# Kernel optimization log

Hardware: AMD Instinct MI355X
Metric: run time of the kernel (lower is better)

The kernel has to match this reference:

```python
import jax, jax.numpy as jnp
import numpy as np

H, D, TS, A, R, TR = 256, 2, 32, 4, 16, 8  # h_size, max_output_degree, t_size, n_aggr, rank, t_rank
BS = 16384


def setup_inputs() -> dict:
    key = jax.random.key(0)
    ks = jax.random.split(key, 9)
    return {
        "neighbour_h": jax.random.normal(ks[0], (BS, D, H), jnp.float32),
        "type_embs": jax.random.normal(ks[1], (BS, TS), jnp.float32),
        # per-child input projections U: (max_output_degree, n_aggr, h_size, rank)
        "U": jax.random.normal(ks[2], (D, A, H, R), jnp.float32) * 0.05,
        "b": jax.random.normal(ks[3], (D, A, 1, R), jnp.float32) * 0.05,
        # type projection
        "U_type": jax.random.normal(ks[4], (TS, A * TR), jnp.float32) * 0.05,
        "b_type": jax.random.normal(ks[5], (1, A * TR), jnp.float32) * 0.05,
        # stacked augmented core tensors T_list: (n_aggr, t_rank+1, rank+1, rank+1, rank)
        "T": jax.random.normal(ks[6], (A, TR + 1, R + 1, R + 1, R), jnp.float32) * 0.02,
        # output projection
        "U_output": jax.random.normal(ks[7], (A, R, H), jnp.float32) * 0.05,
        "b_output": jax.random.normal(ks[8], (A, 1, H), jnp.float32) * 0.05,
    }


def _aug(x):
    # append a constant-1 feature along the last dim: (bs, a, d) -> (bs, a, d+1)
    bs, a, _ = x.shape
    return jnp.concatenate([x, jnp.ones((bs, a, 1), x.dtype)], axis=-1)


def reference(neighbour_h, type_embs, U, b, U_type, b_type, T, U_output, b_output):
    # child projections: (bs, n_ch, n_aggr, rank)
    ch = jnp.einsum('bch,cahr->bcar', neighbour_h, U) + b[:, :, 0, :]
    # type projection: (bs, n_aggr, t_rank)
    tp = (type_embs @ U_type + b_type).reshape(-1, A, TR)
    # augmented (homogeneous) inputs
    h0 = _aug(tp)         # (bs, a, TR+1)
    h1 = _aug(ch[:, 0])   # (bs, a, R+1)
    h2 = _aug(ch[:, 1])   # (bs, a, R+1)
    # sequential multilinear (Tucker/HOSVD) contraction with the core tensor,
    # vectorized over batch and aggregators (original loops over n_aggr)
    r = jnp.einsum('bap,apqrs->baqrs', h0, T)
    r = jnp.einsum('baq,baqrs->bars', h1, r)
    g = jnp.einsum('bar,bars->bas', h2, r)            # (bs, a, R)
    out = jnp.einsum('bar,arh->bah', g, U_output) + b_output[:, 0, :]
    return out.reshape(neighbour_h.shape[0], -1)      # (bs, n_aggr*h_size)
```

## Files before the change

kernel.cpp:

```cpp
#include <hip/hip_runtime.h>

#define NTHR 512
#define TB 32

typedef __attribute__((ext_vector_type(8))) short bf16x8;
typedef __attribute__((ext_vector_type(16))) float f32x16;
typedef __attribute__((ext_vector_type(4))) float f32v4;
typedef float4 f4;
typedef unsigned short u16;

__device__ __forceinline__ u16 f2b(float x) {
  union { float f; unsigned u; } v; v.f = x;
  unsigned r = (v.u + 0x7fffu + ((v.u >> 16) & 1u)) >> 16;
  return (u16)r;
}
__device__ __forceinline__ float b2f(u16 u) {
  union { unsigned u; float f; } v; v.u = ((unsigned)u) << 16;
  return v.f;
}
__device__ __forceinline__ unsigned pack2(float a, float b) {
  return (unsigned)f2b(a) | ((unsigned)f2b(b) << 16);
}
__device__ __forceinline__ unsigned cvtpk(float lo, float hi) {
  unsigned r;
  asm("v_cvt_pk_bf16_f32 %0, %1, %2" : "=v"(r) : "v"(lo), "v"(hi));
  return r;
}
__device__ __forceinline__ f4 ntload4(const float* p) {
  f32v4 v = __builtin_nontemporal_load((const f32v4*)p);
  return make_float4(v.x, v.y, v.z, v.w);
}

#define MFMA32(A, B, C) __builtin_amdgcn_mfma_f32_32x32x16_bf16(A, B, C, 0, 0, 0)

extern "C" __global__ void hosvd_prep(const float* __restrict__ U,
                                      const float* __restrict__ T,
                                      const float* __restrict__ UO,
                                      unsigned* __restrict__ ws32) {
  int id = blockIdx.x * 256 + threadIdx.x;
  if (id < 102400) {
    int j2 = id & 3, frag = id >> 2;
    int l = frag & 63, f2 = frag >> 6;
    int nt = f2 % 5, aks = f2 / 5;
    int ks = aks % 20, a = aks / 20;
    int n = nt * 32 + (l & 31);
    int p = n >> 4, s = n & 15;
    float v[2];
    #pragma unroll
    for (int j = 0; j < 2; ++j) {
      int kp = ks * 16 + (l >> 5) * 8 + j2 * 2 + j;
      int q = (unsigned)kp / 18u, r = kp - q * 18;
      float x = 0.f;
      if (p <= 8 && q <= 16 && r <= 16)
        x = T[(((a * 9 + p) * 17 + q) * 17 + r) * 16 + s];
      v[j] = x;
    }
    ws32[id] = pack2(v[0], v[1]);
  } else if (id < 118784) {
    int rel = id - 102400;
    int j2 = rel & 3, frag = rel >> 2;
    int l = frag & 63, f2 = frag >> 6;
    int nt = f2 & 1, ks = (f2 >> 1) & 15, c = f2 >> 5;
    int n = nt * 32 + (l & 31);
    int a = n >> 4, rr = n & 15;
    int k = ks * 16 + (l >> 5) * 8 + j2 * 2;
    float v0 = U[((c * 4 + a) * 256 + k + 0) * 16 + rr];
    float v1 = U[((c * 4 + a) * 256 + k + 1) * 16 + rr];
    ws32[id] = pack2(v0, v1);
  } else if (id < 126976) {
    int rel = id - 118784;
    int j2 = rel & 3, frag = rel >> 2;
    int l = frag & 63, f2 = frag >> 6;
    int ht = f2 & 7, a = f2 >> 3;
    int h = ht * 32 + (l & 31);
    int k = (l >> 5) * 8 + j2 * 2;
    float v0 = UO[(a * 16 + k + 0) * 256 + h];
    float v1 = UO[(a * 16 + k + 1) * 256 + h];
    ws32[id] = pack2(v0, v1);
  }
}

extern "C" __global__ __launch_bounds__(NTHR, 4)
void hosvd_main(const float* __restrict__ nh, const float* __restrict__ te,
                const float* __restrict__ bw, const float* __restrict__ Ut,
                const float* __restrict__ bt, const float* __restrict__ bO,
                const u16* __restrict__ BTf, const u16* __restrict__ UcTf,
                const u16* __restrict__ UOTf, float* __restrict__ out) {
  __shared__ __align__(16) u16   s_u[20800];
  __shared__ __align__(16) u16   s_ch[TB * 164];
  __shared__ __align__(16) float s_tpt[36 * 32];

  const int t = threadIdx.x;
  const int ib0 = blockIdx.x * TB;
  const int w = t >> 6, l = t & 63;
  const int l31 = l & 31, hi = l >> 5;

  float* UtL = (float*)&s_u[16640];
  float* teL = (float*)&s_u[18688];
  float* s_redf = (float*)s_u;

  if (t < 256) {
    const int row = t >> 3, cc = (t >> 2) & 1, aa = t & 3;
    *(uint2*)&s_ch[row * 164 + cc * 80 + aa * 20 + 16] = make_uint2(0x3F80u, 0u);
  }
  if (t < 128) {
    const int aa = t >> 5, row = t & 31;
    s_tpt[(aa * 9 + 8) * 32 + row] = 1.0f;
  }

  if (t < 256) {
    const int row = t >> 3, k4 = t & 7;
    f4 v = ntload4(&te[(size_t)(ib0 + row) * 32 + k4 * 4]);
    float* d = &teL[row * 33 + k4 * 4];
    d[0] = v.x; d[1] = v.y; d[2] = v.z; d[3] = v.w;
  } else {
    const int j = t - 256;
    *(f4*)&UtL[j * 4] = *(const f4*)&Ut[j * 4];
  }
  for (int lp = t; lp < 4096; lp += NTHR) {
    const int row = lp >> 7, rem = lp & 127;
    const int c = rem >> 6, k0 = (rem & 63) * 4;
    f4 v = ntload4(&nh[((size_t)(ib0 + row) * 2 + c) * 256 + k0]);
    *(uint2*)&s_u[row * 520 + c * 256 + k0] =
        make_uint2(cvtpk(v.x, v.y), cvtpk(v.z, v.w));
  }
  __syncthreads();

  if (w < 4) {
    const int c = w & 1, nt2 = w >> 1;
    f32x16 accC = {0.f, 0.f, 0.f, 0.f, 0.f, 0.f, 0.f, 0.f,
                   0.f, 0.f, 0.f, 0.f, 0.f, 0.f, 0.f, 0.f};
    #pragma unroll
    for (int ks = 0; ks < 16; ++ks) {
      bf16x8 Av = *(const bf16x8*)&s_u[l31 * 520 + c * 256 + ks * 16 + hi * 8];
      bf16x8 Bv = *(const bf16x8*)
          &UcTf[(size_t)(((c * 16 + ks) * 2 + nt2) * 64 + l) * 8];
      accC = MFMA32(Av, Bv, accC);
    }
    const int n = nt2 * 32 + l31;
    const int ca = n >> 4, rr = n & 15;
    const float bias = bw[(c * 4 + ca) * 16 + rr];
    #pragma unroll
    for (int reg = 0; reg < 16; ++reg) {
      const int row = (reg & 3) + 8 * (reg >> 2) + 4 * hi;
      s_ch[row * 164 + c * 80 + ca * 20 + rr] = f2b(accC[reg] + bias);
    }
  } else {
    const int t2 = t - 256;
    const int i = t2 >> 3, off = (t2 & 7) * 4;
    float ac0 = bt[off], ac1 = bt[off + 1], ac2 = bt[off + 2], ac3 = bt[off + 3];
    #pragma unroll
    for (int k = 0; k < 32; ++k) {
      const float tv = teL[i * 33 + k];
      f4 u = *(const f4*)&UtL[k * 32 + off];
      ac0 = fmaf(tv, u.x, ac0);
      ac1 = fmaf(tv, u.y, ac1);
      ac2 = fmaf(tv, u.z, ac2);
      ac3 = fmaf(tv, u.w, ac3);
    }
    #pragma unroll
    for (int jj = 0; jj < 4; ++jj) {
      const int o2 = off + jj;
      const float v = (jj == 0) ? ac0 : (jj == 1) ? ac1 : (jj == 2) ? ac2 : ac3;
      s_tpt[((o2 >> 3) * 9 + (o2 & 7)) * 32 + i] = v;
    }
  }
  __syncthreads();

  {
    const int a = w & 3, kh = w >> 2;
    const u16* h1g = &s_ch[l31 * 164 + a * 20];
    const u16* h2g = h1g + 80;

    f32x16 acc[5];
    #pragma unroll
    for (int nt = 0; nt < 5; ++nt)
      acc[nt] = (f32x16){0.f, 0.f, 0.f, 0.f, 0.f, 0.f, 0.f, 0.f,
                         0.f, 0.f, 0.f, 0.f, 0.f, 0.f, 0.f, 0.f};

    __builtin_amdgcn_s_setprio(1);
    #pragma unroll
    for (int ks2 = 0; ks2 < 10; ++ks2) {
      const int ks = kh * 10 + ks2;
      const u16* bp = &BTf[(size_t)((a * 20 + ks) * 5) * 512 + l * 8];
      bf16x8 B0 = *(const bf16x8*)(bp + 0 * 512);
      bf16x8 B1 = *(const bf16x8*)(bp + 1 * 512);
      bf16x8 B2 = *(const bf16x8*)(bp + 2 * 512);
      bf16x8 B3 = *(const bf16x8*)(bp + 3 * 512);
      bf16x8 B4 = *(const bf16x8*)(bp + 4 * 512);

      const int k0 = ks * 16 + hi * 8;
      const unsigned q0 = (unsigned)k0 / 18u;
      const int r0 = k0 - (int)q0 * 18;
      const int brk = 18 - r0;
      const float h1a = b2f(h1g[q0]);
      const float h1b = b2f(h1g[q0 + 1]);
      float hv[8];
      #pragma unroll
      for (int j = 0; j < 8; ++j) {
        int rr = r0 + j;
        rr = (rr >= 18) ? rr - 18 : rr;
        const float h2v = b2f(h2g[rr]);
        hv[j] = ((j < brk) ? h1a : h1b) * h2v;
      }
      union { unsigned u[4]; bf16x8 v; } Au;
      Au.u[0] = cvtpk(hv[0], hv[1]);
      Au.u[1] = cvtpk(hv[2], hv[3]);
      Au.u[2] = cvtpk(hv[4], hv[5]);
      Au.u[3] = cvtpk(hv[6], hv[7]);

      acc[0] = MFMA32(Au.v, B0, acc[0]);
      acc[1] = MFMA32(Au.v, B1, acc[1]);
      acc[2] = MFMA32(Au.v, B2, acc[2]);
      acc[3] = MFMA32(Au.v, B3, acc[3]);
      acc[4] = MFMA32(Au.v, B4, acc[4]);
    }
    __builtin_amdgcn_s_setprio(0);

    float gp[16];
    #pragma unroll
    for (int reg = 0; reg < 16; ++reg) gp[reg] = 0.f;
    #pragma unroll
    for (int nt = 0; nt < 5; ++nt) {
      int pp = nt * 2 + (l31 >> 4);
      if (pp > 8) pp = 8;
      const float* tpb = &s_tpt[(a * 9 + pp) * 32 + 4 * hi];
      f4 t0 = *(const f4*)&tpb[0];
      f4 t1 = *(const f4*)&tpb[8];
      f4 t2 = *(const f4*)&tpb[16];
      f4 t3 = *(const f4*)&tpb[24];
      gp[0]  = fmaf(t0.x, acc[nt][0],  gp[0]);
      gp[1]  = fmaf(t0.y, acc[nt][1],  gp[1]);
      gp[2]  = fmaf(t0.z, acc[nt][2],  gp[2]);
      gp[3]  = fmaf(t0.w, acc[nt][3],  gp[3]);
      gp[4]  = fmaf(t1.x, acc[nt][4],  gp[4]);
      gp[5]  = fmaf(t1.y, acc[nt][5],  gp[5]);
      gp[6]  = fmaf(t1.z, acc[nt][6],  gp[6]);
      gp[7]  = fmaf(t1.w, acc[nt][7],  gp[7]);
      gp[8]  = fmaf(t2.x, acc[nt][8],  gp[8]);
      gp[9]  = fmaf(t2.y, acc[nt][9],  gp[9]);
      gp[10] = fmaf(t2.z, acc[nt][10], gp[10]);
      gp[11] = fmaf(t2.w, acc[nt][11], gp[11]);
      gp[12] = fmaf(t3.x, acc[nt][12], gp[12]);
      gp[13] = fmaf(t3.y, acc[nt][13], gp[13]);
      gp[14] = fmaf(t3.z, acc[nt][14], gp[14]);
      gp[15] = fmaf(t3.w, acc[nt][15], gp[15]);
    }
    #pragma unroll
    for (int reg = 0; reg < 16; ++reg)
      gp[reg] += __shfl_xor(gp[reg], 16, 64);
    if ((l & 16) == 0) {
      const int s = l & 15;
      #pragma unroll
      for (int reg = 0; reg < 16; ++reg) {
        const int row = (reg & 3) + 8 * (reg >> 2) + 4 * hi;
        s_redf[((kh * 4 + a) * 32 + row) * 16 + s] = gp[reg];
      }
    }
  }
  __syncthreads();

  {
    #pragma unroll
    for (int a = 0; a < 4; ++a) {
      const float* r0p = &s_redf[((0 + a) * 32 + l31) * 16 + hi * 8];
      const float* r1p = &s_redf[((4 + a) * 32 + l31) * 16 + hi * 8];
      f4 xa = *(const f4*)&r0p[0], xb = *(const f4*)&r0p[4];
      f4 ya = *(const f4*)&r1p[0], yb = *(const f4*)&r1p[4];
      union { unsigned u[4]; bf16x8 v; } Au;
      Au.u[0] = cvtpk(xa.x + ya.x, xa.y + ya.y);
      Au.u[1] = cvtpk(xa.z + ya.z, xa.w + ya.w);
      Au.u[2] = cvtpk(xb.x + yb.x, xb.y + yb.y);
      Au.u[3] = cvtpk(xb.z + yb.z, xb.w + yb.w);
      bf16x8 Bv = *(const bf16x8*)&UOTf[((size_t)(a * 8 + w) * 64 + l) * 8];
      const int h = w * 32 + l31;
      const float bias = bO[a * 256 + h];
      f32x16 accE = {bias, bias, bias, bias, bias, bias, bias, bias,
                     bias, bias, bias, bias, bias, bias, bias, bias};
      accE = MFMA32(Au.v, Bv, accE);
      #pragma unroll
      for (int reg = 0; reg < 16; ++reg) {
        const int row = (reg & 3) + 8 * (reg >> 2) + 4 * hi;
        __builtin_nontemporal_store(
            accE[reg], &out[(size_t)(ib0 + row) * 1024 + a * 256 + h]);
      }
    }
  }
}

extern "C" void kernel_launch(void* const* d_in, const int* in_sizes, int n_in,
                              void* d_out, int out_size, void* d_ws, size_t ws_size,
                              hipStream_t stream) {
  const float* nh = (const float*)d_in[0];
  const float* te = (const float*)d_in[1];
  const float* U  = (const float*)d_in[2];
  const float* bw = (const float*)d_in[3];
  const float* Ut = (const float*)d_in[4];
  const float* bt = (const float*)d_in[5];
  const float* T  = (const float*)d_in[6];
  const float* UO = (const float*)d_in[7];
  const float* bO = (const float*)d_in[8];
  float* out = (float*)d_out;

  unsigned* ws32 = (unsigned*)d_ws;
  hipLaunchKernelGGL(hosvd_prep, dim3(496), dim3(256), 0, stream, U, T, UO, ws32);

  const u16* BTf  = (const u16*)d_ws;
  const u16* UcTf = BTf + 204800;
  const u16* UOTf = UcTf + 32768;

  const int bs = in_sizes[0] / 512;
  hipLaunchKernelGGL(hosvd_main, dim3(bs / TB), dim3(NTHR), 0, stream,
                     nh, te, bw, Ut, bt, bO, BTf, UcTf, UOTf, out);
}
```

Baseline: 39.49 us.

## Process two batch tiles per block with register prefetch of second tile

Each block now handles two 32-row tiles (the second offset by half the batch), halving the grid. After the first tile's projection phase, the second tile's neighbour and type inputs are loaded into registers so the global load latency overlaps the first tile's core contraction and output stage. Launch bounds drop from 4 to 2 blocks per SM to make room for the 8 extra float4 prefetch registers. This trades occupancy and grid parallelism (256 blocks) for latency hiding.

After: 79.74 us. +101.9%, slower.

```diff
diff --git a/kernel.cpp b/kernel.cpp
--- a/kernel.cpp
+++ b/kernel.cpp
@@ -80,18 +80,18 @@
   }
 }
 
-extern "C" __global__ __launch_bounds__(NTHR, 4)
+extern "C" __global__ __launch_bounds__(NTHR, 2)
 void hosvd_main(const float* __restrict__ nh, const float* __restrict__ te,
                 const float* __restrict__ bw, const float* __restrict__ Ut,
                 const float* __restrict__ bt, const float* __restrict__ bO,
                 const u16* __restrict__ BTf, const u16* __restrict__ UcTf,
-                const u16* __restrict__ UOTf, float* __restrict__ out) {
+                const u16* __restrict__ UOTf, float* __restrict__ out,
+                int half) {
   __shared__ __align__(16) u16   s_u[20800];
   __shared__ __align__(16) u16   s_ch[TB * 164];
   __shared__ __align__(16) float s_tpt[36 * 32];
 
   const int t = threadIdx.x;
-  const int ib0 = blockIdx.x * TB;
   const int w = t >> 6, l = t & 63;
   const int l31 = l & 31, hi = l >> 5;
 
@@ -108,183 +108,221 @@
     s_tpt[(aa * 9 + 8) * 32 + row] = 1.0f;
   }
 
-  if (t < 256) {
-    const int row = t >> 3, k4 = t & 7;
-    f4 v = ntload4(&te[(size_t)(ib0 + row) * 32 + k4 * 4]);
-    float* d = &teL[row * 33 + k4 * 4];
-    d[0] = v.x; d[1] = v.y; d[2] = v.z; d[3] = v.w;
-  } else {
-    const int j = t - 256;
-    *(f4*)&UtL[j * 4] = *(const f4*)&Ut[j * 4];
-  }
-  for (int lp = t; lp < 4096; lp += NTHR) {
-    const int row = lp >> 7, rem = lp & 127;
-    const int c = rem >> 6, k0 = (rem & 63) * 4;
-    f4 v = ntload4(&nh[((size_t)(ib0 + row) * 2 + c) * 256 + k0]);
-    *(uint2*)&s_u[row * 520 + c * 256 + k0] =
-        make_uint2(cvtpk(v.x, v.y), cvtpk(v.z, v.w));
-  }
-  __syncthreads();
-
-  if (w < 4) {
-    const int c = w & 1, nt2 = w >> 1;
-    f32x16 accC = {0.f, 0.f, 0.f, 0.f, 0.f, 0.f, 0.f, 0.f,
-                   0.f, 0.f, 0.f, 0.f, 0.f, 0.f, 0.f, 0.f};
-    #pragma unroll
-    for (int ks = 0; ks < 16; ++ks) {
-      bf16x8 Av = *(const bf16x8*)&s_u[l31 * 520 + c * 256 + ks * 16 + hi * 8];
-      bf16x8 Bv = *(const bf16x8*)
-          &UcTf[(size_t)(((c * 16 + ks) * 2 + nt2) * 64 + l) * 8];
-      accC = MFMA32(Av, Bv, accC);
-    }
-    const int n = nt2 * 32 + l31;
-    const int ca = n >> 4, rr = n & 15;
-    const float bias = bw[(c * 4 + ca) * 16 + rr];
-    #pragma unroll
-    for (int reg = 0; reg < 16; ++reg) {
-      const int row = (reg & 3) + 8 * (reg >> 2) + 4 * hi;
-      s_ch[row * 164 + c * 80 + ca * 20 + rr] = f2b(accC[reg] + bias);
-    }
-  } else {
-    const int t2 = t - 256;
-    const int i = t2 >> 3, off = (t2 & 7) * 4;
-    float ac0 = bt[off], ac1 = bt[off + 1], ac2 = bt[off + 2], ac3 = bt[off + 3];
-    #pragma unroll
-    for (int k = 0; k < 32; ++k) {
-      const float tv = teL[i * 33 + k];
-      f4 u = *(const f4*)&UtL[k * 32 + off];
-      ac0 = fmaf(tv, u.x, ac0);
-      ac1 = fmaf(tv, u.y, ac1);
-      ac2 = fmaf(tv, u.z, ac2);
-      ac3 = fmaf(tv, u.w, ac3);
-    }
-    #pragma unroll
-    for (int jj = 0; jj < 4; ++jj) {
-      const int o2 = off + jj;
-      const float v = (jj == 0) ? ac0 : (jj == 1) ? ac1 : (jj == 2) ? ac2 : ac3;
-      s_tpt[((o2 >> 3) * 9 + (o2 & 7)) * 32 + i] = v;
-    }
-  }
-  __syncthreads();
-
-  {
-    const int a = w & 3, kh = w >> 2;
-    const u16* h1g = &s_ch[l31 * 164 + a * 20];
-    const u16* h2g = h1g + 80;
-
-    f32x16 acc[5];
-    #pragma unroll
-    for (int nt = 0; nt < 5; ++nt)
-      acc[nt] = (f32x16){0.f, 0.f, 0.f, 0.f, 0.f, 0.f, 0.f, 0.f,
-                         0.f, 0.f, 0.f, 0.f, 0.f, 0.f, 0.f, 0.f};
-
-    __builtin_amdgcn_s_setprio(1);
-    #pragma unroll
-    for (int ks2 = 0; ks2 < 10; ++ks2) {
-      const int ks = kh * 10 + ks2;
-      const u16* bp = &BTf[(size_t)((a * 20 + ks) * 5) * 512 + l * 8];
-      bf16x8 B0 = *(const bf16x8*)(bp + 0 * 512);
-      bf16x8 B1 = *(const bf16x8*)(bp + 1 * 512);
-      bf16x8 B2 = *(const bf16x8*)(bp + 2 * 512);
-      bf16x8 B3 = *(const bf16x8*)(bp + 3 * 512);
-      bf16x8 B4 = *(const bf16x8*)(bp + 4 * 512);
-
-      const int k0 = ks * 16 + hi * 8;
-      const unsigned q0 = (unsigned)k0 / 18u;
-      const int r0 = k0 - (int)q0 * 18;
-      const int brk = 18 - r0;
-      const float h1a = b2f(h1g[q0]);
-      const float h1b = b2f(h1g[q0 + 1]);
-      float hv[8];
-      #pragma unroll
-      for (int j = 0; j < 8; ++j) {
-        int rr = r0 + j;
-        rr = (rr >= 18) ? rr - 18 : rr;
-        const float h2v = b2f(h2g[rr]);
-        hv[j] = ((j < brk) ? h1a : h1b) * h2v;
-      }
-      union { unsigned u[4]; bf16x8 v; } Au;
-      Au.u[0] = cvtpk(hv[0], hv[1]);
-      Au.u[1] = cvtpk(hv[2], hv[3]);
-      Au.u[2] = cvtpk(hv[4], hv[5]);
-      Au.u[3] = cvtpk(hv[6], hv[7]);
-
-      acc[0] = MFMA32(Au.v, B0, acc[0]);
-      acc[1] = MFMA32(Au.v, B1, acc[1]);
-      acc[2] = MFMA32(Au.v, B2, acc[2]);
-      acc[3] = MFMA32(Au.v, B3, acc[3]);
-      acc[4] = MFMA32(Au.v, B4, acc[4]);
-    }
-    __builtin_amdgcn_s_setprio(0);
-
-    float gp[16];
-    #pragma unroll
-    for (int reg = 0; reg < 16; ++reg) gp[reg] = 0.f;
-    #pragma unroll
-    for (int nt = 0; nt < 5; ++nt) {
-      int pp = nt * 2 + (l31 >> 4);
-      if (pp > 8) pp = 8;
-      const float* tpb = &s_tpt[(a * 9 + pp) * 32 + 4 * hi];
-      f4 t0 = *(const f4*)&tpb[0];
-      f4 t1 = *(const f4*)&tpb[8];
-      f4 t2 = *(const f4*)&tpb[16];
-      f4 t3 = *(const f4*)&tpb[24];
-      gp[0]  = fmaf(t0.x, acc[nt][0],  gp[0]);
-      gp[1]  = fmaf(t0.y, acc[nt][1],  gp[1]);
-      gp[2]  = fmaf(t0.z, acc[nt][2],  gp[2]);
-      gp[3]  = fmaf(t0.w, acc[nt][3],  gp[3]);
-      gp[4]  = fmaf(t1.x, acc[nt][4],  gp[4]);
-      gp[5]  = fmaf(t1.y, acc[nt][5],  gp[5]);
-      gp[6]  = fmaf(t1.z, acc[nt][6],  gp[6]);
-      gp[7]  = fmaf(t1.w, acc[nt][7],  gp[7]);
-      gp[8]  = fmaf(t2.x, acc[nt][8],  gp[8]);
-      gp[9]  = fmaf(t2.y, acc[nt][9],  gp[9]);
-      gp[10] = fmaf(t2.z, acc[nt][10], gp[10]);
-      gp[11] = fmaf(t2.w, acc[nt][11], gp[11]);
-      gp[12] = fmaf(t3.x, acc[nt][12], gp[12]);
-      gp[13] = fmaf(t3.y, acc[nt][13], gp[13]);
-      gp[14] = fmaf(t3.z, acc[nt][14], gp[14]);
-      gp[15] = fmaf(t3.w, acc[nt][15], gp[15]);
-    }
-    #pragma unroll
-    for (int reg = 0; reg < 16; ++reg)
-      gp[reg] += __shfl_xor(gp[reg], 16, 64);
-    if ((l & 16) == 0) {
-      const int s = l & 15;
+  f4 Rnh[8];
+  f4 Rte;
+
+  for (int it = 0; it < 2; ++it) {
+    const int ib0 = blockIdx.x * TB + it * half;
+
+    if (it == 0) {
+      if (t < 256) {
+        const int row = t >> 3, k4 = t & 7;
+        f4 v = ntload4(&te[(size_t)(ib0 + row) * 32 + k4 * 4]);
+        float* d = &teL[row * 33 + k4 * 4];
+        d[0] = v.x; d[1] = v.y; d[2] = v.z; d[3] = v.w;
+      } else {
+        const int j = t - 256;
+        *(f4*)&UtL[j * 4] = *(const f4*)&Ut[j * 4];
+      }
+      for (int lp = t; lp < 4096; lp += NTHR) {
+        const int row = lp >> 7, rem = lp & 127;
+        const int c = rem >> 6, k0 = (rem & 63) * 4;
+        f4 v = ntload4(&nh[((size_t)(ib0 + row) * 2 + c) * 256 + k0]);
+        *(uint2*)&s_u[row * 520 + c * 256 + k0] =
+            make_uint2(cvtpk(v.x, v.y), cvtpk(v.z, v.w));
+      }
+    } else {
+      if (t < 256) {
+        const int row = t >> 3, k4 = t & 7;
+        float* d = &teL[row * 33 + k4 * 4];
+        d[0] = Rte.x; d[1] = Rte.y; d[2] = Rte.z; d[3] = Rte.w;
+      }
+      #pragma unroll
+      for (int k2 = 0; k2 < 8; ++k2) {
+        const int lp = t + k2 * NTHR;
+        const int row = lp >> 7, rem = lp & 127;
+        const int c = rem >> 6, k0 = (rem & 63) * 4;
+        f4 v = Rnh[k2];
+        *(uint2*)&s_u[row * 520 + c * 256 + k0] =
+            make_uint2(cvtpk(v.x, v.y), cvtpk(v.z, v.w));
+      }
+    }
+    __syncthreads();
+
+    if (w < 4) {
+      const int c = w & 1, nt2 = w >> 1;
+      f32x16 accC = {0.f, 0.f, 0.f, 0.f, 0.f, 0.f, 0.f, 0.f,
+                     0.f, 0.f, 0.f, 0.f, 0.f, 0.f, 0.f, 0.f};
+      #pragma unroll
+      for (int ks = 0; ks < 16; ++ks) {
+        bf16x8 Av = *(const bf16x8*)&s_u[l31 * 520 + c * 256 + ks * 16 + hi * 8];
+        bf16x8 Bv = *(const bf16x8*)
+            &UcTf[(size_t)(((c * 16 + ks) * 2 + nt2) * 64 + l) * 8];
+        accC = MFMA32(Av, Bv, accC);
+      }
+      const int n = nt2 * 32 + l31;
+      const int ca = n >> 4, rr = n & 15;
+      const float bias = bw[(c * 4 + ca) * 16 + rr];
       #pragma unroll
       for (int reg = 0; reg < 16; ++reg) {
         const int row = (reg & 3) + 8 * (reg >> 2) + 4 * hi;
-        s_redf[((kh * 4 + a) * 32 + row) * 16 + s] = gp[reg];
-      }
-    }
-  }
-  __syncthreads();
-
-  {
-    #pragma unroll
-    for (int a = 0; a < 4; ++a) {
-      const float* r0p = &s_redf[((0 + a) * 32 + l31) * 16 + hi * 8];
-      const float* r1p = &s_redf[((4 + a) * 32 + l31) * 16 + hi * 8];
-      f4 xa = *(const f4*)&r0p[0], xb = *(const f4*)&r0p[4];
-      f4 ya = *(const f4*)&r1p[0], yb = *(const f4*)&r1p[4];
-      union { unsigned u[4]; bf16x8 v; } Au;
-      Au.u[0] = cvtpk(xa.x + ya.x, xa.y + ya.y);
-      Au.u[1] = cvtpk(xa.z + ya.z, xa.w + ya.w);
-      Au.u[2] = cvtpk(xb.x + yb.x, xb.y + yb.y);
-      Au.u[3] = cvtpk(xb.z + yb.z, xb.w + yb.w);
-      bf16x8 Bv = *(const bf16x8*)&UOTf[((size_t)(a * 8 + w) * 64 + l) * 8];
-      const int h = w * 32 + l31;
-      const float bias = bO[a * 256 + h];
-      f32x16 accE = {bias, bias, bias, bias, bias, bias, bias, bias,
-                     bias, bias, bias, bias, bias, bias, bias, bias};
-      accE = MFMA32(Au.v, Bv, accE);
-      #pragma unroll
-      for (int reg = 0; reg < 16; ++reg) {
-        const int row = (reg & 3) + 8 * (reg >> 2) + 4 * hi;
-        __builtin_nontemporal_store(
-            accE[reg], &out[(size_t)(ib0 + row) * 1024 + a * 256 + h]);
-      }
-    }
+        s_ch[row * 164 + c * 80 + ca * 20 + rr] = f2b(accC[reg] + bias);
+      }
+    } else {
+      const int t2 = t - 256;
+      const int i = t2 >> 3, off = (t2 & 7) * 4;
+      float ac0 = bt[off], ac1 = bt[off + 1], ac2 = bt[off + 2], ac3 = bt[off + 3];
+      #pragma unroll
+      for (int k = 0; k < 32; ++k) {
+        const float tv = teL[i * 33 + k];
+        f4 u = *(const f4*)&UtL[k * 32 + off];
+        ac0 = fmaf(tv, u.x, ac0);
+        ac1 = fmaf(tv, u.y, ac1);
+        ac2 = fmaf(tv, u.z, ac2);
+        ac3 = fmaf(tv, u.w, ac3);
+      }
+      #pragma unroll
+      for (int jj = 0; jj < 4; ++jj) {
+        const int o2 = off + jj;
+        const float v = (jj == 0) ? ac0 : (jj == 1) ? ac1 : (jj == 2) ? ac2 : ac3;
+        s_tpt[((o2 >> 3) * 9 + (o2 & 7)) * 32 + i] = v;
+      }
+    }
+    __syncthreads();
+
+    if (it == 0) {
+      const int ib1 = blockIdx.x * TB + half;
+      #pragma unroll
+      for (int k2 = 0; k2 < 8; ++k2) {
+        const int lp = t + k2 * NTHR;
+        const int row = lp >> 7, rem = lp & 127;
+        const int c = rem >> 6, k0 = (rem & 63) * 4;
+        Rnh[k2] = ntload4(&nh[((size_t)(ib1 + row) * 2 + c) * 256 + k0]);
+      }
+      if (t < 256)
+        Rte = ntload4(&te[(size_t)(ib1 + (t >> 3)) * 32 + (t & 7) * 4]);
+    }
+
+    {
+      const int a = w & 3, kh = w >> 2;
+      const u16* h1g = &s_ch[l31 * 164 + a * 20];
+      const u16* h2g = h1g + 80;
+
+      f32x16 acc[5];
+      #pragma unroll
+      for (int nt = 0; nt < 5; ++nt)
+        acc[nt] = (f32x16){0.f, 0.f, 0.f, 0.f, 0.f, 0.f, 0.f, 0.f,
+                           0.f, 0.f, 0.f, 0.f, 0.f, 0.f, 0.f, 0.f};
+
+      __builtin_amdgcn_s_setprio(1);
+      #pragma unroll
+      for (int ks2 = 0; ks2 < 10; ++ks2) {
+        const int ks = kh * 10 + ks2;
+        const u16* bp = &BTf[(size_t)((a * 20 + ks) * 5) * 512 + l * 8];
+        bf16x8 B0 = *(const bf16x8*)(bp + 0 * 512);
+        bf16x8 B1 = *(const bf16x8*)(bp + 1 * 512);
+        bf16x8 B2 = *(const bf16x8*)(bp + 2 * 512);
+        bf16x8 B3 = *(const bf16x8*)(bp + 3 * 512);
+        bf16x8 B4 = *(const bf16x8*)(bp + 4 * 512);
+
+        const int k0 = ks * 16 + hi * 8;
+        const unsigned q0 = (unsigned)k0 / 18u;
+        const int r0 = k0 - (int)q0 * 18;
+        const int brk = 18 - r0;
+        const float h1a = b2f(h1g[q0]);
+        const float h1b = b2f(h1g[q0 + 1]);
+        float hv[8];
+        #pragma unroll
+        for (int j = 0; j < 8; ++j) {
+          int rr = r0 + j;
+          rr = (rr >= 18) ? rr - 18 : rr;
+          const float h2v = b2f(h2g[rr]);
+          hv[j] = ((j < brk) ? h1a : h1b) * h2v;
+        }
+        union { unsigned u[4]; bf16x8 v; } Au;
+        Au.u[0] = cvtpk(hv[0], hv[1]);
+        Au.u[1] = cvtpk(hv[2], hv[3]);
+        Au.u[2] = cvtpk(hv[4], hv[5]);
+        Au.u[3] = cvtpk(hv[6], hv[7]);
+
+        acc[0] = MFMA32(Au.v, B0, acc[0]);
+        acc[1] = MFMA32(Au.v, B1, acc[1]);
+        acc[2] = MFMA32(Au.v, B2, acc[2]);
+        acc[3] = MFMA32(Au.v, B3, acc[3]);
+        acc[4] = MFMA32(Au.v, B4, acc[4]);
+      }
+      __builtin_amdgcn_s_setprio(0);
+
+      float gp[16];
+      #pragma unroll
+      for (int reg = 0; reg < 16; ++reg) gp[reg] = 0.f;
+      #pragma unroll
+      for (int nt = 0; nt < 5; ++nt) {
+        int pp = nt * 2 + (l31 >> 4);
+        if (pp > 8) pp = 8;
+        const float* tpb = &s_tpt[(a * 9 + pp) * 32 + 4 * hi];
+        f4 t0 = *(const f4*)&tpb[0];
+        f4 t1 = *(const f4*)&tpb[8];
+        f4 t2 = *(const f4*)&tpb[16];
+        f4 t3 = *(const f4*)&tpb[24];
+        gp[0]  = fmaf(t0.x, acc[nt][0],  gp[0]);
+        gp[1]  = fmaf(t0.y, acc[nt][1],  gp[1]);
+        gp[2]  = fmaf(t0.z, acc[nt][2],  gp[2]);
+        gp[3]  = fmaf(t0.w, acc[nt][3],  gp[3]);
+        gp[4]  = fmaf(t1.x, acc[nt][4],  gp[4]);
+        gp[5]  = fmaf(t1.y, acc[nt][5],  gp[5]);
+        gp[6]  = fmaf(t1.z, acc[nt][6],  gp[6]);
+        gp[7]  = fmaf(t1.w, acc[nt][7],  gp[7]);
+        gp[8]  = fmaf(t2.x, acc[nt][8],  gp[8]);
+        gp[9]  = fmaf(t2.y, acc[nt][9],  gp[9]);
+        gp[10] = fmaf(t2.z, acc[nt][10], gp[10]);
+        gp[11] = fmaf(t2.w, acc[nt][11], gp[11]);
+        gp[12] = fmaf(t3.x, acc[nt][12], gp[12]);
+        gp[13] = fmaf(t3.y, acc[nt][13], gp[13]);
+        gp[14] = fmaf(t3.z, acc[nt][14], gp[14]);
+        gp[15] = fmaf(t3.w, acc[nt][15], gp[15]);
+      }
+      #pragma unroll
+      for (int reg = 0; reg < 16; ++reg)
+        gp[reg] += __shfl_xor(gp[reg], 16, 64);
+      if ((l & 16) == 0) {
+        const int s = l & 15;
+        #pragma unroll
+        for (int reg = 0; reg < 16; ++reg) {
+          const int row = (reg & 3) + 8 * (reg >> 2) + 4 * hi;
+          s_redf[((kh * 4 + a) * 32 + row) * 16 + s] = gp[reg];
+        }
+      }
+    }
+    __syncthreads();
+
+    {
+      #pragma unroll
+      for (int a = 0; a < 4; ++a) {
+        const float* r0p = &s_redf[((0 + a) * 32 + l31) * 16 + hi * 8];
+        const float* r1p = &s_redf[((4 + a) * 32 + l31) * 16 + hi * 8];
+        f4 xa = *(const f4*)&r0p[0], xb = *(const f4*)&r0p[4];
+        f4 ya = *(const f4*)&r1p[0], yb = *(const f4*)&r1p[4];
+        union { unsigned u[4]; bf16x8 v; } Au;
+        Au.u[0] = cvtpk(xa.x + ya.x, xa.y + ya.y);
+        Au.u[1] = cvtpk(xa.z + ya.z, xa.w + ya.w);
+        Au.u[2] = cvtpk(xb.x + yb.x, xb.y + yb.y);
+        Au.u[3] = cvtpk(xb.z + yb.z, xb.w + yb.w);
+        bf16x8 Bv = *(const bf16x8*)&UOTf[((size_t)(a * 8 + w) * 64 + l) * 8];
+        const int h = w * 32 + l31;
+        const float bias = bO[a * 256 + h];
+        f32x16 accE = {bias, bias, bias, bias, bias, bias, bias, bias,
+                       bias, bias, bias, bias, bias, bias, bias, bias};
+        accE = MFMA32(Au.v, Bv, accE);
+        #pragma unroll
+        for (int reg = 0; reg < 16; ++reg) {
+          const int row = (reg & 3) + 8 * (reg >> 2) + 4 * hi;
+          __builtin_nontemporal_store(
+              accE[reg], &out[(size_t)(ib0 + row) * 1024 + a * 256 + h]);
+        }
+      }
+    }
+    if (it == 0) __syncthreads();
   }
 }
 
@@ -310,6 +348,7 @@
   const u16* UOTf = UcTf + 32768;
 
   const int bs = in_sizes[0] / 512;
-  hipLaunchKernelGGL(hosvd_main, dim3(bs / TB), dim3(NTHR), 0, stream,
-                     nh, te, bw, Ut, bt, bO, BTf, UcTf, UOTf, out);
-}
+  const int half = bs / 2;
+  hipLaunchKernelGGL(hosvd_main, dim3(half / TB), dim3(NTHR), 0, stream,
+                     nh, te, bw, Ut, bt, bO, BTf, UcTf, UOTf, out, half);
+}
```
